# Optimization experiments

Measured on AMD Instinct MI355X. Metric: run time of the kernel, lower is better.

Reference implementation:

```python
import jax, jax.numpy as jnp
import numpy as np

EPS = 1e-5        # BatchNorm1d default eps
SLOPE = 0.01      # torch LeakyReLU default negative slope


def setup_inputs() -> dict:
    key = jax.random.key(0)
    ks = jax.random.split(key, 10)
    N3, N2, N1, N0 = 4096, 16384, 65536, 262144  # coarse -> fine point hierarchy
    return {
        "feats": jax.random.normal(ks[0], (N3, 258), jnp.float32),
        "skip1": jax.random.normal(ks[1], (N0, 128), jnp.float32),
        "skip2": jax.random.normal(ks[2], (N1, 256), jnp.float32),
        "skip3": jax.random.normal(ks[3], (N2, 512), jnp.float32),
        "idx1": jax.random.randint(ks[4], (N2,), 0, N3, jnp.int32),
        "idx2": jax.random.randint(ks[5], (N1,), 0, N2, jnp.int32),
        "idx3": jax.random.randint(ks[6], (N0,), 0, N1, jnp.int32),
        "W1": jax.random.normal(ks[7], (770, 129), jnp.float32) * 0.05,
        "b1": jnp.zeros((129,), jnp.float32),
        "g1": jnp.ones((129,), jnp.float32),
        "be1": jnp.zeros((129,), jnp.float32),
        "W2": jax.random.normal(ks[8], (385, 64), jnp.float32) * 0.05,
        "b2": jnp.zeros((64,), jnp.float32),
        "g2": jnp.ones((64,), jnp.float32),
        "be2": jnp.zeros((64,), jnp.float32),
        "W3": jax.random.normal(ks[9], (192, 34), jnp.float32) * 0.05,
        "b3": jnp.zeros((34,), jnp.float32),
    }


def _bn(y, g, b):
    # training-mode batch norm over the points dimension (biased variance)
    m = y.mean(axis=0)
    v = y.var(axis=0)
    return (y - m) * jax.lax.rsqrt(v + EPS) * g + b


def _lrelu(x):
    return jnp.where(x >= 0, x, SLOPE * x)


def reference(feats, skip1, skip2, skip3, idx1, idx2, idx3,
              W1, b1, g1, be1, W2, b2, g2, be2, W3, b3):
    # stage 1: nearest upsample N3->N2, concat skip3, conv1x1 + BN + LeakyReLU
    x = jnp.concatenate([feats[idx1], skip3], axis=1)        # [N2, 770]
    x = _lrelu(_bn(x @ W1 + b1, g1, be1))                    # [N2, 129]
    # stage 2: upsample N2->N1
    x = jnp.concatenate([x[idx2], skip2], axis=1)            # [N1, 385]
    x = _lrelu(_bn(x @ W2 + b2, g2, be2))                    # [N1, 64]
    # stage 3: upsample N1->N0, plain conv1x1 (no BN / no activation)
    x = jnp.concatenate([x[idx3], skip1], axis=1)            # [N0, 192]
    return x @ W3 + b3                                       # [N0, 34]
```

## Files before the change

kernel.cpp:

```cpp
#include <hip/hip_runtime.h>

#define EPS 1e-5f
#define SLOPE 0.01f

typedef __attribute__((ext_vector_type(4))) float f32x4;
typedef __attribute__((ext_vector_type(8))) short bf16x8;

__device__ __forceinline__ short f2bf(float f) {
    unsigned u = __float_as_uint(f);
    unsigned r = (u + 0x7FFFu + ((u >> 16) & 1u)) >> 16;
    return (short)r;
}
__device__ __forceinline__ float lrelu(float v) { return v >= 0.f ? v : SLOPE * v; }

__device__ __forceinline__ void gload16(const float* g, float* l) {
    __builtin_amdgcn_global_load_lds(
        (const __attribute__((address_space(1))) unsigned*)g,
        (__attribute__((address_space(3))) unsigned*)l, 16, 0, 0);
}
__device__ __forceinline__ void gload4(const float* g, float* l) {
    __builtin_amdgcn_global_load_lds(
        (const __attribute__((address_space(1))) unsigned*)g,
        (__attribute__((address_space(3))) unsigned*)l, 4, 0, 0);
}
__device__ __forceinline__ void wait_vm(int n) {
    switch (n) {
    case 0:  asm volatile("s_waitcnt vmcnt(0)" ::: "memory"); break;
    case 4:  asm volatile("s_waitcnt vmcnt(4)" ::: "memory"); break;
    case 16: asm volatile("s_waitcnt vmcnt(16)" ::: "memory"); break;
    default: asm volatile("s_waitcnt vmcnt(0)" ::: "memory"); break;
    }
}

__global__ void prep(const float* __restrict__ W1, const float* __restrict__ W2,
                     const float* __restrict__ W3,
                     short* __restrict__ Wt1, short* __restrict__ Wt2,
                     short* __restrict__ Wt3, float* __restrict__ stats)
{
    int id = blockIdx.x * 256 + threadIdx.x;
    if (id < 2048) stats[id] = 0.f;
    {
        if (id < 115200) {
            int e = id & 7, lane = (id >> 3) & 63, g = id >> 9;
            int t = g / 9, nt = g - t * 9;
            int kv = t * 32 + (lane >> 4) * 8 + e;
            int n  = nt * 16 + (lane & 15);
            float v = 0.f; int ks = -1;
            if (kv < 258) ks = kv; else if (kv >= 288) ks = kv - 30;
            if (ks >= 0 && n < 129) v = W1[ks * 129 + n];
            Wt1[id] = f2bf(v);
        }
    }
    {
        if (id < 28672) {
            int e = id & 7, lane = (id >> 3) & 63, g = id >> 9;
            int t = g >> 2, nt = g & 3;
            int kv = t * 32 + (lane >> 4) * 8 + e;
            int n  = nt * 16 + (lane & 15);
            float v = 0.f; int ks = -1;
            if (kv < 129) ks = kv; else if (kv >= 192) ks = kv - 63;
            if (ks >= 0) v = W2[ks * 64 + n];
            Wt2[id] = f2bf(v);
        }
    }
    {
        if (id < 9216) {
            int e = id & 7, lane = (id >> 3) & 63, g = id >> 9;
            int t = g / 3, nt = g - t * 3;
            int kv = t * 32 + (lane >> 4) * 8 + e;
            int n  = nt * 16 + (lane & 15);
            float v = (n < 34) ? W3[kv * 34 + n] : 0.f;
            Wt3[id] = f2bf(v);
        }
    }
}

template<int XD, int XVALID, int XTILES, int SD, int NT, int NVALID, int OD,
         bool XA16, bool BN, bool STATS, int MINW>
__global__ __launch_bounds__(256, MINW)
void mfma_stage(const float* __restrict__ xsrc, const float* __restrict__ skip,
                const int* __restrict__ idx, const short* __restrict__ Wt,
                const float* __restrict__ bias,
                const float* __restrict__ bnsc, const float* __restrict__ bnsh,
                float* __restrict__ out, float* __restrict__ ssum,
                float* __restrict__ ssq)
{
    constexpr int NCX = XVALID / 64;
    constexpr int NCS = SD / 64;
    constexpr int NC  = NCX + NCS;
    constexpr bool HASPART = (XVALID % 64) != 0;
    constexpr int NPAD = NT * 16;

    __shared__ __align__(16) float abuf[4][2][1024];

    const int tid  = threadIdx.x;
    const int wave = tid >> 6, lane = tid & 63;
    const int lr = lane & 15;
    const int kg = lane >> 4;
    const int row0w = (blockIdx.x * 4 + wave) * 16;
    const short* wtf = Wt + (lane << 3);

    const float* prow[4];
    if (XA16) {
#pragma unroll
        for (int q = 0; q < 4; ++q)
            prow[q] = xsrc + (size_t)idx[row0w + q * 4 + (lane >> 4)] * XD;
    }

    f32x4 acc[NT];
#pragma unroll
    for (int nt = 0; nt < NT; ++nt) acc[nt] = (f32x4){0.f, 0.f, 0.f, 0.f};

    if (HASPART) {
        const float* xr = xsrc + (size_t)idx[row0w + lr] * XD;
        constexpr int kb = (XTILES - 1) * 32;
        float v[8];
#pragma unroll
        for (int e = 0; e < 8; ++e) {
            int ks = kb + kg * 8 + e;
            float f = 0.f;
            if (ks < XVALID) {
                f = xr[ks];
                if (BN) f = lrelu(fmaf(f, bnsc[ks], bnsh[ks]));
            }
            v[e] = f;
        }
        bf16x8 a;
#pragma unroll
        for (int e = 0; e < 8; ++e) a[e] = f2bf(v[e]);
#pragma unroll
        for (int nt = 0; nt < NT; ++nt) {
            bf16x8 b = *(const bf16x8*)(wtf + (((XTILES - 1) * NT + nt) << 9));
            acc[nt] = __builtin_amdgcn_mfma_f32_16x16x32_bf16(a, b, acc[nt], 0, 0, 0);
        }
    }

    auto issue = [&](int c) {
        float* wb = &abuf[wave][c & 1][0];
        if (c < NCX) {
            if (XA16) {
#pragma unroll
                for (int q = 0; q < 4; ++q) {
                    const int rl = q * 4 + (lane >> 4);
                    const int s  = lane & 15;
                    const int cf = (s & ~7) | ((s & 7) ^ (rl & 6));
                    gload16(prow[q] + c * 64 + cf * 4, wb + q * 256);
                }
            } else {
#pragma unroll
                for (int j = 0; j < 16; ++j) {
                    const float* rp = xsrc + (size_t)idx[row0w + j] * XD;
                    const int s  = lane >> 2;
                    const int cf = (s & ~7) | ((s & 7) ^ (j & 6));
                    gload4(rp + c * 64 + cf * 4 + (lane & 3), wb + j * 64);
                }
            }
        } else {
            const int jc = c - NCX;
#pragma unroll
            for (int q = 0; q < 4; ++q) {
                const int rl = q * 4 + (lane >> 4);
                const int s  = lane & 15;
                const int cf = (s & ~7) | ((s & 7) ^ (rl & 6));
                gload16(skip + (size_t)(row0w + rl) * SD + jc * 64 + cf * 4,
                        wb + q * 256);
            }
        }
    };

    issue(0);

#pragma unroll
    for (int c = 0; c < NC; ++c) {
        bf16x8 Bf[2][NT];
#pragma unroll
        for (int tt = 0; tt < 2; ++tt) {
            const int tv = (c < NCX) ? (2 * c + tt) : (XTILES + 2 * (c - NCX) + tt);
#pragma unroll
            for (int nt = 0; nt < NT; ++nt)
                Bf[tt][nt] = *(const bf16x8*)(wtf + ((tv * NT + nt) << 9));
        }
        if (c + 1 < NC) issue(c + 1);
        wait_vm((c + 1 < NC) ? (((c + 1) < NCX && !XA16) ? 16 : 4) : 0);

        const float* wb = &abuf[wave][c & 1][0];
#pragma unroll
        for (int tt = 0; tt < 2; ++tt) {
            const int s0 = tt * 8 + kg * 2;
            const int sw = (s0 & ~7) | ((s0 & 7) ^ (lr & 6));
            const float* fp = wb + lr * 64 + sw * 4;
            f32x4 lo = *(const f32x4*)fp;
            f32x4 hi = *(const f32x4*)(fp + 4);
            float v[8];
#pragma unroll
            for (int e = 0; e < 4; ++e) { v[e] = lo[e]; v[e + 4] = hi[e]; }
            if (BN && c < NCX) {
                const int kb = c * 64 + tt * 32 + kg * 8;
                f32x4 c0 = *(const f32x4*)(bnsc + kb);
                f32x4 c1 = *(const f32x4*)(bnsc + kb + 4);
                f32x4 h0 = *(const f32x4*)(bnsh + kb);
                f32x4 h1 = *(const f32x4*)(bnsh + kb + 4);
#pragma unroll
                for (int e = 0; e < 4; ++e) {
                    v[e]     = lrelu(fmaf(v[e],     c0[e], h0[e]));
                    v[e + 4] = lrelu(fmaf(v[e + 4], c1[e], h1[e]));
                }
            }
            bf16x8 a;
#pragma unroll
            for (int e = 0; e < 8; ++e) a[e] = f2bf(v[e]);
#pragma unroll
            for (int nt = 0; nt < NT; ++nt)
                acc[nt] = __builtin_amdgcn_mfma_f32_16x16x32_bf16(a, Bf[tt][nt],
                                                                  acc[nt], 0, 0, 0);
        }
    }

#pragma unroll
    for (int nt = 0; nt < NT; ++nt) {
        const int n = nt * 16 + lr;
        const float bv = (n < NVALID) ? bias[n] : 0.f;
#pragma unroll
        for (int r = 0; r < 4; ++r) acc[nt][r] += bv;
        if (n < NVALID) {
#pragma unroll
            for (int r = 0; r < 4; ++r)
                out[(size_t)(row0w + kg * 4 + r) * OD + n] = acc[nt][r];
        }
    }

    if (STATS) {
        float* ls = &abuf[0][0][0];
        __syncthreads();
        for (int i = tid; i < 2 * NPAD; i += 256) ls[i] = 0.f;
        __syncthreads();
#pragma unroll
        for (int nt = 0; nt < NT; ++nt) {
            float s = acc[nt][0] + acc[nt][1] + acc[nt][2] + acc[nt][3];
            float q = acc[nt][0]*acc[nt][0] + acc[nt][1]*acc[nt][1]
                    + acc[nt][2]*acc[nt][2] + acc[nt][3]*acc[nt][3];
            s += __shfl_xor(s, 16, 64);
            s += __shfl_xor(s, 32, 64);
            q += __shfl_xor(q, 16, 64);
            q += __shfl_xor(q, 32, 64);
            if (lane < 16) {
                atomicAdd(&ls[nt * 16 + lr], s);
                atomicAdd(&ls[NPAD + nt * 16 + lr], q);
            }
        }
        __syncthreads();
        for (int i = tid; i < NPAD; i += 256) {
            atomicAdd(&ssum[i], ls[i]);
            atomicAdd(&ssq[i], ls[NPAD + i]);
        }
    }
}

__global__ void finalize_bn(const float* __restrict__ sum,
                            const float* __restrict__ sq,
                            const float* __restrict__ g,
                            const float* __restrict__ be,
                            float* __restrict__ scale,
                            float* __restrict__ shift,
                            int C, int CPAD, float invN)
{
    int c = blockIdx.x * blockDim.x + threadIdx.x;
    if (c < CPAD) {
        if (c < C) {
            float m   = sum[c] * invN;
            float var = fmaf(-m, m, sq[c] * invN);
            float rs  = rsqrtf(var + EPS);
            float sc  = rs * g[c];
            scale[c] = sc;
            shift[c] = fmaf(-m, sc, be[c]);
        } else {
            scale[c] = 0.f;
            shift[c] = 0.f;
        }
    }
}

extern "C" void kernel_launch(void* const* d_in, const int* in_sizes, int n_in,
                              void* d_out, int out_size, void* d_ws, size_t ws_size,
                              hipStream_t stream) {
    const float* feats = (const float*)d_in[0];
    const float* skip1 = (const float*)d_in[1];
    const float* skip2 = (const float*)d_in[2];
    const float* skip3 = (const float*)d_in[3];
    const int*   idx1  = (const int*)d_in[4];
    const int*   idx2  = (const int*)d_in[5];
    const int*   idx3  = (const int*)d_in[6];
    const float* W1    = (const float*)d_in[7];
    const float* b1    = (const float*)d_in[8];
    const float* g1    = (const float*)d_in[9];
    const float* be1   = (const float*)d_in[10];
    const float* W2    = (const float*)d_in[11];
    const float* b2    = (const float*)d_in[12];
    const float* g2    = (const float*)d_in[13];
    const float* be2   = (const float*)d_in[14];
    const float* W3    = (const float*)d_in[15];
    const float* b3    = (const float*)d_in[16];

    float* ws   = (float*)d_ws;
    float* sum1 = ws;        float* sq1 = ws + 256;
    float* sc1  = ws + 512;  float* sh1 = ws + 768;
    float* sum2 = ws + 1024; float* sq2 = ws + 1280;
    float* sc2  = ws + 1536; float* sh2 = ws + 1792;
    short* Wt1  = (short*)(ws + 2048);
    short* Wt2  = Wt1 + 115200;
    short* Wt3  = Wt2 + 28672;
    float* y1   = ws + 2048 + (115200 + 28672 + 9216) / 2;
    float* y2   = y1 + 16384 * 192;
    float* outp = (float*)d_out;

    prep<<<450, 256, 0, stream>>>(W1, W2, W3, Wt1, Wt2, Wt3, ws);

    mfma_stage<258, 258, 9, 512, 9, 129, 192, false, false, true, 1>
        <<<256, 256, 0, stream>>>(feats, skip3, idx1, Wt1, b1,
                                  nullptr, nullptr, y1, sum1, sq1);
    finalize_bn<<<1, 256, 0, stream>>>(sum1, sq1, g1, be1, sc1, sh1,
                                       129, 192, 1.f / 16384.f);

    mfma_stage<192, 192, 6, 256, 4, 64, 64, true, true, true, 4>
        <<<1024, 256, 0, stream>>>(y1, skip2, idx2, Wt2, b2,
                                   sc1, sh1, y2, sum2, sq2);
    finalize_bn<<<1, 256, 0, stream>>>(sum2, sq2, g2, be2, sc2, sh2,
                                       64, 64, 1.f / 65536.f);

    mfma_stage<64, 64, 2, 128, 3, 34, 34, true, true, false, 4>
        <<<4096, 256, 0, stream>>>(y2, skip1, idx3, Wt3, b3,
                                   sc2, sh2, outp, nullptr, nullptr);
}
```

Baseline: 127.1 us.

## Triple-buffer LDS pipeline with deeper prefetch, LDS-cached BN params, preloaded weights

Moves the per-wave LDS staging from double to triple buffering. Loads are issued two chunks ahead, and the vmcnt waits are computed to match. Weight fragments are prefetched ahead, or preloaded entirely for the small last stage, and BN scale/shift are staged in LDS. The separate partial-tile path for stage 1 is dropped by padding W1's K to a full 64-chunk with clamped column reads. Hoisting the gather row pointers adds registers and LDS, so minimum waves per SIMD drops from 4 to 3, which may cut occupancy.

```diff
diff --git a/kernel.cpp b/kernel.cpp
--- a/kernel.cpp
+++ b/kernel.cpp
@@ -23,11 +23,18 @@
         (const __attribute__((address_space(1))) unsigned*)g,
         (__attribute__((address_space(3))) unsigned*)l, 4, 0, 0);
 }
+
+#define WCASE(N) case N: asm volatile("s_waitcnt vmcnt(" #N ")" ::: "memory"); break;
 __device__ __forceinline__ void wait_vm(int n) {
     switch (n) {
-    case 0:  asm volatile("s_waitcnt vmcnt(0)" ::: "memory"); break;
-    case 4:  asm volatile("s_waitcnt vmcnt(4)" ::: "memory"); break;
-    case 16: asm volatile("s_waitcnt vmcnt(16)" ::: "memory"); break;
+    WCASE(0) WCASE(1) WCASE(2) WCASE(3) WCASE(4) WCASE(5) WCASE(6) WCASE(7)
+    WCASE(8) WCASE(9) WCASE(10) WCASE(11) WCASE(12) WCASE(13) WCASE(14) WCASE(15)
+    WCASE(16) WCASE(17) WCASE(18) WCASE(19) WCASE(20) WCASE(21) WCASE(22) WCASE(23)
+    WCASE(24) WCASE(25) WCASE(26) WCASE(27) WCASE(28) WCASE(29) WCASE(30) WCASE(31)
+    WCASE(32) WCASE(33) WCASE(34) WCASE(35) WCASE(36) WCASE(37) WCASE(38) WCASE(39)
+    WCASE(40) WCASE(41) WCASE(42) WCASE(43) WCASE(44) WCASE(45) WCASE(46) WCASE(47)
+    WCASE(48) WCASE(49) WCASE(50) WCASE(51) WCASE(52) WCASE(53) WCASE(54) WCASE(55)
+    WCASE(56) WCASE(57) WCASE(58) WCASE(59) WCASE(60) WCASE(61) WCASE(62) WCASE(63)
     default: asm volatile("s_waitcnt vmcnt(0)" ::: "memory"); break;
     }
 }
@@ -39,44 +46,38 @@
 {
     int id = blockIdx.x * 256 + threadIdx.x;
     if (id < 2048) stats[id] = 0.f;
-    {
-        if (id < 115200) {
-            int e = id & 7, lane = (id >> 3) & 63, g = id >> 9;
-            int t = g / 9, nt = g - t * 9;
-            int kv = t * 32 + (lane >> 4) * 8 + e;
-            int n  = nt * 16 + (lane & 15);
-            float v = 0.f; int ks = -1;
-            if (kv < 258) ks = kv; else if (kv >= 288) ks = kv - 30;
-            if (ks >= 0 && n < 129) v = W1[ks * 129 + n];
-            Wt1[id] = f2bf(v);
-        }
-    }
-    {
-        if (id < 28672) {
-            int e = id & 7, lane = (id >> 3) & 63, g = id >> 9;
-            int t = g >> 2, nt = g & 3;
-            int kv = t * 32 + (lane >> 4) * 8 + e;
-            int n  = nt * 16 + (lane & 15);
-            float v = 0.f; int ks = -1;
-            if (kv < 129) ks = kv; else if (kv >= 192) ks = kv - 63;
-            if (ks >= 0) v = W2[ks * 64 + n];
-            Wt2[id] = f2bf(v);
-        }
-    }
-    {
-        if (id < 9216) {
-            int e = id & 7, lane = (id >> 3) & 63, g = id >> 9;
-            int t = g / 3, nt = g - t * 3;
-            int kv = t * 32 + (lane >> 4) * 8 + e;
-            int n  = nt * 16 + (lane & 15);
-            float v = (n < 34) ? W3[kv * 34 + n] : 0.f;
-            Wt3[id] = f2bf(v);
-        }
-    }
-}
-
-template<int XD, int XVALID, int XTILES, int SD, int NT, int NVALID, int OD,
-         bool XA16, bool BN, bool STATS, int MINW>
+    if (id < 26 * 9 * 512) {
+        int e = id & 7, lane = (id >> 3) & 63, g = id >> 9;
+        int t = g / 9, nt = g - t * 9;
+        int kv = t * 32 + (lane >> 4) * 8 + e;
+        int n  = nt * 16 + (lane & 15);
+        float v = 0.f; int ks = -1;
+        if (kv < 258) ks = kv; else if (kv >= 320) ks = kv - 62;
+        if (ks >= 0 && n < 129) v = W1[ks * 129 + n];
+        Wt1[id] = f2bf(v);
+    }
+    if (id < 14 * 4 * 512) {
+        int e = id & 7, lane = (id >> 3) & 63, g = id >> 9;
+        int t = g >> 2, nt = g & 3;
+        int kv = t * 32 + (lane >> 4) * 8 + e;
+        int n  = nt * 16 + (lane & 15);
+        float v = 0.f; int ks = -1;
+        if (kv < 129) ks = kv; else if (kv >= 192) ks = kv - 63;
+        if (ks >= 0) v = W2[ks * 64 + n];
+        Wt2[id] = f2bf(v);
+    }
+    if (id < 6 * 3 * 512) {
+        int e = id & 7, lane = (id >> 3) & 63, g = id >> 9;
+        int t = g / 3, nt = g - t * 3;
+        int kv = t * 32 + (lane >> 4) * 8 + e;
+        int n  = nt * 16 + (lane & 15);
+        float v = (n < 34) ? W3[kv * 34 + n] : 0.f;
+        Wt3[id] = f2bf(v);
+    }
+}
+
+template<int XD, int SD, int NCX, int NCS, int NT, int NVALID, int OD,
+         bool XA16, int XCLAMP, bool BN, bool STATS, bool PRELB, int MINW>
 __global__ __launch_bounds__(256, MINW)
 void mfma_stage(const float* __restrict__ xsrc, const float* __restrict__ skip,
                 const int* __restrict__ idx, const short* __restrict__ Wt,
@@ -85,13 +86,12 @@
                 float* __restrict__ out, float* __restrict__ ssum,
                 float* __restrict__ ssq)
 {
-    constexpr int NCX = XVALID / 64;
-    constexpr int NCS = SD / 64;
-    constexpr int NC  = NCX + NCS;
-    constexpr bool HASPART = (XVALID % 64) != 0;
+    constexpr int NC = NCX + NCS;
+    constexpr int T = 2 * NC;
     constexpr int NPAD = NT * 16;
 
-    __shared__ __align__(16) float abuf[4][2][1024];
+    __shared__ __align__(16) float abuf[4][3][1024];
+    __shared__ __align__(16) float bnl[BN ? 2 * NCX * 64 : 4];
 
     const int tid  = threadIdx.x;
     const int wave = tid >> 6, lane = tid & 63;
@@ -100,48 +100,39 @@
     const int row0w = (blockIdx.x * 4 + wave) * 16;
     const short* wtf = Wt + (lane << 3);
 
+    if (BN) {
+        for (int i = tid; i < NCX * 64; i += 256) {
+            bnl[i] = bnsc[i];
+            bnl[NCX * 64 + i] = bnsh[i];
+        }
+        __syncthreads();
+    }
+
     const float* prow[4];
+    const float* rp16[16];
     if (XA16) {
 #pragma unroll
         for (int q = 0; q < 4; ++q)
-            prow[q] = xsrc + (size_t)idx[row0w + q * 4 + (lane >> 4)] * XD;
+            prow[q] = xsrc + (size_t)idx[row0w + q * 4 + kg] * XD;
+    } else {
+#pragma unroll
+        for (int j = 0; j < 16; ++j)
+            rp16[j] = xsrc + (size_t)idx[row0w + j] * XD;
     }
 
     f32x4 acc[NT];
 #pragma unroll
     for (int nt = 0; nt < NT; ++nt) acc[nt] = (f32x4){0.f, 0.f, 0.f, 0.f};
 
-    if (HASPART) {
-        const float* xr = xsrc + (size_t)idx[row0w + lr] * XD;
-        constexpr int kb = (XTILES - 1) * 32;
-        float v[8];
-#pragma unroll
-        for (int e = 0; e < 8; ++e) {
-            int ks = kb + kg * 8 + e;
-            float f = 0.f;
-            if (ks < XVALID) {
-                f = xr[ks];
-                if (BN) f = lrelu(fmaf(f, bnsc[ks], bnsh[ks]));
-            }
-            v[e] = f;
-        }
-        bf16x8 a;
-#pragma unroll
-        for (int e = 0; e < 8; ++e) a[e] = f2bf(v[e]);
-#pragma unroll
-        for (int nt = 0; nt < NT; ++nt) {
-            bf16x8 b = *(const bf16x8*)(wtf + (((XTILES - 1) * NT + nt) << 9));
-            acc[nt] = __builtin_amdgcn_mfma_f32_16x16x32_bf16(a, b, acc[nt], 0, 0, 0);
-        }
-    }
+    auto sopsf = [](int c) { return (c < NCX && !XA16) ? 16 : 4; };
 
     auto issue = [&](int c) {
-        float* wb = &abuf[wave][c & 1][0];
+        float* wb = &abuf[wave][c % 3][0];
         if (c < NCX) {
             if (XA16) {
 #pragma unroll
                 for (int q = 0; q < 4; ++q) {
-                    const int rl = q * 4 + (lane >> 4);
+                    const int rl = q * 4 + kg;
                     const int s  = lane & 15;
                     const int cf = (s & ~7) | ((s & 7) ^ (rl & 6));
                     gload16(prow[q] + c * 64 + cf * 4, wb + q * 256);
@@ -149,17 +140,18 @@
             } else {
 #pragma unroll
                 for (int j = 0; j < 16; ++j) {
-                    const float* rp = xsrc + (size_t)idx[row0w + j] * XD;
                     const int s  = lane >> 2;
                     const int cf = (s & ~7) | ((s & 7) ^ (j & 6));
-                    gload4(rp + c * 64 + cf * 4 + (lane & 3), wb + j * 64);
+                    int col = c * 64 + cf * 4 + (lane & 3);
+                    if (XCLAMP > 0 && c == NCX - 1) col = min(col, XCLAMP - 1);
+                    gload4(rp16[j] + col, wb + j * 64);
                 }
             }
         } else {
             const int jc = c - NCX;
 #pragma unroll
             for (int q = 0; q < 4; ++q) {
-                const int rl = q * 4 + (lane >> 4);
+                const int rl = q * 4 + kg;
                 const int s  = lane & 15;
                 const int cf = (s & ~7) | ((s & 7) ^ (rl & 6));
                 gload16(skip + (size_t)(row0w + rl) * SD + jc * 64 + cf * 4,
@@ -168,22 +160,45 @@
         }
     };
 
+    bf16x8 Bp[PRELB ? T * NT : 1];
+    bf16x8 Bf[PRELB ? 1 : 3][2][NT];
+
+    if (PRELB) {
+#pragma unroll
+        for (int tv = 0; tv < T; ++tv)
+#pragma unroll
+            for (int nt = 0; nt < NT; ++nt)
+                Bp[tv * NT + nt] = *(const bf16x8*)(wtf + ((tv * NT + nt) << 9));
+    }
+
     issue(0);
+    if (NC > 1) issue(1);
+
+    if (!PRELB) {
+#pragma unroll
+        for (int tt = 0; tt < 2; ++tt)
+#pragma unroll
+            for (int nt = 0; nt < NT; ++nt) {
+                Bf[0][tt][nt] = *(const bf16x8*)(wtf + ((tt * NT + nt) << 9));
+                if (NC > 1)
+                    Bf[1][tt][nt] = *(const bf16x8*)(wtf + (((2 + tt) * NT + nt) << 9));
+            }
+    }
 
 #pragma unroll
     for (int c = 0; c < NC; ++c) {
-        bf16x8 Bf[2][NT];
-#pragma unroll
-        for (int tt = 0; tt < 2; ++tt) {
-            const int tv = (c < NCX) ? (2 * c + tt) : (XTILES + 2 * (c - NCX) + tt);
-#pragma unroll
-            for (int nt = 0; nt < NT; ++nt)
-                Bf[tt][nt] = *(const bf16x8*)(wtf + ((tv * NT + nt) << 9));
-        }
-        if (c + 1 < NC) issue(c + 1);
-        wait_vm((c + 1 < NC) ? (((c + 1) < NCX && !XA16) ? 16 : 4) : 0);
-
-        const float* wb = &abuf[wave][c & 1][0];
+        if (c + 2 < NC) issue(c + 2);
+        wait_vm(((c + 1 < NC) ? sopsf(c + 1) : 0) + ((c + 2 < NC) ? sopsf(c + 2) : 0));
+        if (!PRELB && c + 2 < NC) {
+#pragma unroll
+            for (int tt = 0; tt < 2; ++tt)
+#pragma unroll
+                for (int nt = 0; nt < NT; ++nt)
+                    Bf[(c + 2) % 3][tt][nt] =
+                        *(const bf16x8*)(wtf + (((2 * (c + 2) + tt) * NT + nt) << 9));
+        }
+
+        const float* wb = &abuf[wave][c % 3][0];
 #pragma unroll
         for (int tt = 0; tt < 2; ++tt) {
             const int s0 = tt * 8 + kg * 2;
@@ -196,10 +211,10 @@
             for (int e = 0; e < 4; ++e) { v[e] = lo[e]; v[e + 4] = hi[e]; }
             if (BN && c < NCX) {
                 const int kb = c * 64 + tt * 32 + kg * 8;
-                f32x4 c0 = *(const f32x4*)(bnsc + kb);
-                f32x4 c1 = *(const f32x4*)(bnsc + kb + 4);
-                f32x4 h0 = *(const f32x4*)(bnsh + kb);
-                f32x4 h1 = *(const f32x4*)(bnsh + kb + 4);
+                f32x4 c0 = *(const f32x4*)&bnl[kb];
+                f32x4 c1 = *(const f32x4*)&bnl[kb + 4];
+                f32x4 h0 = *(const f32x4*)&bnl[NCX * 64 + kb];
+                f32x4 h1 = *(const f32x4*)&bnl[NCX * 64 + kb + 4];
 #pragma unroll
                 for (int e = 0; e < 4; ++e) {
                     v[e]     = lrelu(fmaf(v[e],     c0[e], h0[e]));
@@ -210,9 +225,12 @@
 #pragma unroll
             for (int e = 0; e < 8; ++e) a[e] = f2bf(v[e]);
 #pragma unroll
-            for (int nt = 0; nt < NT; ++nt)
-                acc[nt] = __builtin_amdgcn_mfma_f32_16x16x32_bf16(a, Bf[tt][nt],
-                                                                  acc[nt], 0, 0, 0);
+            for (int nt = 0; nt < NT; ++nt) {
+                bf16x8 b;
+                if (PRELB) b = Bp[(2 * c + tt) * NT + nt];
+                else       b = Bf[c % 3][tt][nt];
+                acc[nt] = __builtin_amdgcn_mfma_f32_16x16x32_bf16(a, b, acc[nt], 0, 0, 0);
+            }
         }
     }
 
@@ -307,27 +325,27 @@
     float* sum2 = ws + 1024; float* sq2 = ws + 1280;
     float* sc2  = ws + 1536; float* sh2 = ws + 1792;
     short* Wt1  = (short*)(ws + 2048);
-    short* Wt2  = Wt1 + 115200;
+    short* Wt2  = Wt1 + 119808;
     short* Wt3  = Wt2 + 28672;
-    float* y1   = ws + 2048 + (115200 + 28672 + 9216) / 2;
+    float* y1   = ws + 2048 + (119808 + 28672 + 9216) / 2;
     float* y2   = y1 + 16384 * 192;
     float* outp = (float*)d_out;
 
-    prep<<<450, 256, 0, stream>>>(W1, W2, W3, Wt1, Wt2, Wt3, ws);
-
-    mfma_stage<258, 258, 9, 512, 9, 129, 192, false, false, true, 1>
+    prep<<<468, 256, 0, stream>>>(W1, W2, W3, Wt1, Wt2, Wt3, ws);
+
+    mfma_stage<258, 512, 5, 8, 9, 129, 192, false, 258, false, true, false, 1>
         <<<256, 256, 0, stream>>>(feats, skip3, idx1, Wt1, b1,
                                   nullptr, nullptr, y1, sum1, sq1);
     finalize_bn<<<1, 256, 0, stream>>>(sum1, sq1, g1, be1, sc1, sh1,
                                        129, 192, 1.f / 16384.f);
 
-    mfma_stage<192, 192, 6, 256, 4, 64, 64, true, true, true, 4>
+    mfma_stage<192, 256, 3, 4, 4, 64, 64, true, 0, true, true, false, 3>
         <<<1024, 256, 0, stream>>>(y1, skip2, idx2, Wt2, b2,
                                    sc1, sh1, y2, sum2, sq2);
     finalize_bn<<<1, 256, 0, stream>>>(sum2, sq2, g2, be2, sc2, sh2,
                                        64, 64, 1.f / 65536.f);
 
-    mfma_stage<64, 64, 2, 128, 3, 34, 34, true, true, false, 4>
+    mfma_stage<64, 128, 1, 2, 3, 34, 34, true, 0, true, false, true, 3>
         <<<4096, 256, 0, stream>>>(y2, skip1, idx3, Wt3, b3,
                                    sc2, sh2, outp, nullptr, nullptr);
 }
```

Measured after the change: 122.5 us. 3.7% less time.
